# Optimization experiments

Hardware: AMD Instinct MI355X
Metric: run time of the kernel (lower is better)

The kernel has to match this reference:

```python
import jax, jax.numpy as jnp
import numpy as np

B, DIM, NX, NY = 4, 64, 256, 256
HEADS, DIM_HEAD, LATENT, DIM_OUT, KM = 4, 32, 128, 64, 2
DH = DIM_HEAD * KM  # LowRankKernel head dim (also RoPE dim) = 64
EPS = 1e-5
MIN_FREQ = 1.0 / 64.0  # RotaryEmbedding default in FactFormer/LNS repo


def _gelu(x):
    return jax.nn.gelu(x, approximate=False)  # torch nn.GELU default (erf)


def _conv1x1(u, w):
    # u: [b,c,h,w], w: [out,c]  (1x1 conv == channel matmul)
    return jnp.einsum('bchw,oc->bohw', u, w)


def _pooling_reducer(x, win, ln_g, ln_b, w1, w2, b2):
    # x: [b, n_keep, n_pool, c] -> Linear, mean-pool over n_pool, LN+FFN
    h = jnp.einsum('bnmc,hc->bnmh', x, win).mean(axis=2)  # [b, n, hid]
    m = h.mean(axis=-1, keepdims=True)
    v = h.var(axis=-1, keepdims=True)
    h = (h - m) / jnp.sqrt(v + EPS) * ln_g + ln_b
    return _gelu(h @ w1.T) @ w2.T + b2  # [b, n, latent]


def _rope_freqs(n):
    pos = jnp.linspace(0.0, 1.0, n) / MIN_FREQ  # scale/min_freq = 64
    inv = 1.0 / (10000.0 ** (jnp.arange(0, DH, 2, dtype=jnp.float32) / DH))
    f = pos[:, None] * inv[None, :]            # [n, DH//2]
    return jnp.concatenate([f, f], axis=-1)    # [n, DH]


def _apply_rope(x, f):
    # rotate_half = cat(-x2, x1) on half-split (FactFormer convention)
    d = x.shape[-1] // 2
    rot = jnp.concatenate([-x[..., d:], x[..., :d]], axis=-1)
    return x * jnp.cos(f) + rot * jnp.sin(f)


def _low_rank_kernel(x, wqk):
    # x: [b, n, latent] -> K: [b, heads, n, n]; scaling=1, dropout=Identity, qk_norm=False
    b, n, _ = x.shape
    qk = x @ wqk.T
    q, k = jnp.split(qk, 2, axis=-1)
    q = q.reshape(b, n, HEADS, DH).transpose(0, 2, 1, 3)
    k = k.reshape(b, n, HEADS, DH).transpose(0, 2, 1, 3)
    f = _rope_freqs(n)
    q = _apply_rope(q, f)
    k = _apply_rope(k, f)
    return jnp.einsum('bhid,bhjd->bhij', q, k)


def _forward(u, gn_w, gn_b, w_in_proj, w_to_in,
             px_win, px_ln_g, px_ln_b, px_w1, px_w2, px_b2,
             py_win, py_ln_g, py_ln_b, py_w1, py_w2, py_b2,
             kx_wqk, ky_wqk, out_w1, out_w2):
    # GroupNorm(1, dim): normalize over (C,H,W) per sample, affine
    m = u.mean(axis=(1, 2, 3), keepdims=True)
    v = u.var(axis=(1, 2, 3), keepdims=True)
    un = (u - m) / jnp.sqrt(v + EPS) * gn_w[None, :, None, None] + gn_b[None, :, None, None]
    u_phi = _conv1x1(un, w_in_proj)  # [b, heads*dim_head, nx, ny]
    ui = _conv1x1(un, w_to_in)       # [b, dim, nx, ny]
    # to_x: pool over ny -> tokens along nx; to_y: pool over nx -> tokens along ny
    ux = _pooling_reducer(ui.transpose(0, 2, 3, 1), px_win, px_ln_g, px_ln_b, px_w1, px_w2, px_b2)  # [b, nx, latent]
    uy = _pooling_reducer(ui.transpose(0, 3, 2, 1), py_win, py_ln_g, py_ln_b, py_w1, py_w2, py_b2)  # [b, ny, latent]
    kx = _low_rank_kernel(ux, kx_wqk)  # [b, h, nx, nx]
    ky = _low_rank_kernel(uy, ky_wqk)  # [b, h, ny, ny]
    b, hc, nx, ny = u_phi.shape
    up = u_phi.reshape(b, HEADS, hc // HEADS, nx, ny)
    up = jnp.einsum('bhij,bhcjm->bhcim', kx, up)
    up = jnp.einsum('bhlm,bhcim->bhcil', ky, up)
    up = up.reshape(b, hc, nx, ny)
    # InstanceNorm2d (no affine, no running stats)
    m2 = up.mean(axis=(2, 3), keepdims=True)
    v2 = up.var(axis=(2, 3), keepdims=True)
    upn = (up - m2) / jnp.sqrt(v2 + EPS)
    out = _conv1x1(_gelu(_conv1x1(upn, out_w1)), out_w2)
    return out + u


def setup_inputs() -> dict:
    key = jax.random.key(0)
    ks = jax.random.split(key, 16)
    def w(k, shape, s=0.02):
        return (jax.random.normal(k, shape) * s).astype(jnp.float32)
    return {
        'u': jax.random.normal(ks[0], (B, DIM, NX, NY), dtype=jnp.float32),
        'gn_w': jnp.ones((DIM,), jnp.float32), 'gn_b': jnp.zeros((DIM,), jnp.float32),
        'w_in_proj': w(ks[1], (HEADS * DIM_HEAD, DIM)),
        'w_to_in': w(ks[2], (DIM, DIM)),
        'px_win': w(ks[3], (DIM, DIM)),
        'px_ln_g': jnp.ones((DIM,), jnp.float32), 'px_ln_b': jnp.zeros((DIM,), jnp.float32),
        'px_w1': w(ks[4], (2 * DIM, DIM)), 'px_w2': w(ks[5], (LATENT, 2 * DIM)),
        'px_b2': jnp.zeros((LATENT,), jnp.float32),
        'py_win': w(ks[6], (DIM, DIM)),
        'py_ln_g': jnp.ones((DIM,), jnp.float32), 'py_ln_b': jnp.zeros((DIM,), jnp.float32),
        'py_w1': w(ks[7], (2 * DIM, DIM)), 'py_w2': w(ks[8], (LATENT, 2 * DIM)),
        'py_b2': jnp.zeros((LATENT,), jnp.float32),
        'kx_wqk': w(ks[9], (2 * HEADS * DH, LATENT)),
        'ky_wqk': w(ks[10], (2 * HEADS * DH, LATENT)),
        'out_w1': w(ks[11], (DIM_OUT, HEADS * DIM_HEAD)),
        'out_w2': w(ks[12], (DIM_OUT, DIM_OUT)),
    }


def reference(u, gn_w, gn_b, w_in_proj, w_to_in,
              px_win, px_ln_g, px_ln_b, px_w1, px_w2, px_b2,
              py_win, py_ln_g, py_ln_b, py_w1, py_w2, py_b2,
              kx_wqk, ky_wqk, out_w1, out_w2):
    return _forward(u, gn_w, gn_b, w_in_proj, w_to_in,
                    px_win, px_ln_g, px_ln_b, px_w1, px_w2, px_b2,
                    py_win, py_ln_g, py_ln_b, py_w1, py_w2, py_b2,
                    kx_wqk, ky_wqk, out_w1, out_w2)
```

## Files before the change

kernel.cpp:

```cpp
#include <hip/hip_runtime.h>
#include <math.h>

typedef unsigned short ushort_t;
typedef unsigned int uint_t;
typedef __attribute__((ext_vector_type(8))) short s8v;
typedef __attribute__((ext_vector_type(4))) float f4;

#define NPIX 65536
#define EPS_ 1e-5f

__device__ __forceinline__ float bf2f(ushort_t u){ return __uint_as_float(((uint_t)u)<<16); }
__device__ __forceinline__ ushort_t f2bf(float f){
  uint_t u = __float_as_uint(f);
  uint_t r = (u + 0x7fffu + ((u>>16)&1u)) >> 16;
  return (ushort_t)r;
}
__device__ __forceinline__ float bflo(uint_t p){ return __uint_as_float(p<<16); }
__device__ __forceinline__ float bfhi(uint_t p){ return __uint_as_float(p & 0xffff0000u); }
__device__ __forceinline__ uint_t packbf(float a, float b){ return (uint_t)f2bf(a) | ((uint_t)f2bf(b)<<16); }

__device__ __forceinline__ f4 MFMA(s8v a, s8v b, f4 c){
  return __builtin_amdgcn_mfma_f32_16x16x32_bf16(a, b, c, 0, 0, 0);
}

__device__ __forceinline__ float wave_sum(float v){
  #pragma unroll
  for(int m=32;m>=1;m>>=1) v += __shfl_xor(v, m, 64);
  return v;
}

__global__ __launch_bounds__(256) void k1_stats(const float* __restrict__ u,
    float* __restrict__ part, float* __restrict__ pc, float* __restrict__ poolx){
  int blk = blockIdx.x; int b = blk>>8; int c = (blk>>2)&63; int iq = blk&3;
  int t = threadIdx.x; int lane = t&63; int w = t>>6;
  const float* up = u + ((size_t)(b*64+c))*NPIX + iq*64*256;
  __shared__ float red[8];
  float cs=0.f, ss=0.f;
  for(int r=0;r<64;r++){
    float v = up[r*256 + t];
    cs += v; ss += v*v;
  }
  pc[((b*64+c)*4 + iq)*256 + t] = cs;
  float a1 = wave_sum(cs), a2 = wave_sum(ss);
  if(lane==0){ red[w]=a1; red[4+w]=a2; }
  __syncthreads();
  if(t==0){
    part[((b*64+c)*4+iq)*2]   = red[0]+red[1]+red[2]+red[3];
    part[((b*64+c)*4+iq)*2+1] = red[4]+red[5]+red[6]+red[7];
  }
  int r = t>>2, ck = t&3;
  const float* rp = up + r*256 + ck*64;
  float s=0.f;
  #pragma unroll 4
  for(int j=0;j<16;j++){
    float4 v4 = *(const float4*)(rp + j*4);
    s += v4.x + v4.y + v4.z + v4.w;
  }
  s += __shfl_xor(s, 1, 64);
  s += __shfl_xor(s, 2, 64);
  if(ck==0) poolx[(b*256 + iq*64 + r)*64 + c] = s * (1.f/256.f);
}

__global__ void k2_fin(const float* __restrict__ part, float* __restrict__ gnmv){
  int t = threadIdx.x; int b = t>>6; int i = t&63;
  float S1=0.f, S2=0.f;
  #pragma unroll
  for(int q=0;q<4;q++){
    S1 += part[((b*64+i)*4+q)*2];
    S2 += part[((b*64+i)*4+q)*2+1];
  }
  S1 = wave_sum(S1); S2 = wave_sum(S2);
  if(i==0){
    const float inv = 1.f/4194304.f;
    float m = S1*inv; float v = S2*inv - m*m;
    gnmv[b*2] = m; gnmv[b*2+1] = rsqrtf(v + EPS_);
  }
}

__global__ __launch_bounds__(256) void k2b_pool(const float* __restrict__ pc,
    float* __restrict__ pooly){
  int blk = blockIdx.x; int b = blk>>6; int c = blk&63;
  int t = threadIdx.x;
  const float* p = pc + ((size_t)(b*64+c))*4*256 + t;
  float s = p[0] + p[256] + p[512] + p[768];
  pooly[(b*256+t)*64 + c] = s * (1.f/256.f);
}

__global__ __launch_bounds__(256) void k8a_fold(const float* __restrict__ gnmv,
    const float* __restrict__ gnw, const float* __restrict__ gnb,
    const float* __restrict__ w_in_proj, const float* __restrict__ out_w2,
    ushort_t* __restrict__ wpb, float* __restrict__ c0g, ushort_t* __restrict__ w2b){
  int b = blockIdx.x; int t = threadIdx.x;
  __shared__ float scs[64], shs[64];
  if(t<64){
    float mean = gnmv[b*2], rstd = gnmv[b*2+1];
    float sc = rstd*gnw[t];
    scs[t] = sc; shs[t] = gnb[t] - mean*sc;
  }
  __syncthreads();
  int oc = t>>1, h = t&1;
  float c0 = 0.f;
  for(int k=0;k<32;k++){
    int ch = h*32 + k;
    float wv = w_in_proj[oc*64 + ch];
    wpb[((size_t)b*128 + oc)*64 + ch] = f2bf(wv*scs[ch]);
    c0 += wv*shs[ch];
  }
  c0 += __shfl_xor(c0, 1, 64);
  if(h==0) c0g[b*128 + oc] = c0;
  if(b==0){
    for(int e=t;e<4096;e+=256) w2b[e] = f2bf(out_w2[e]);
  }
}

__global__ void k8b_fold(const float* __restrict__ istat,
    const float* __restrict__ out_w1, ushort_t* __restrict__ W1b,
    float* __restrict__ bias1){
  int b = blockIdx.x; int t = threadIdx.x;
  __shared__ float ms[128], rss[128];
  ms[t] = istat[(b*128+t)*2];       rss[t] = istat[(b*128+t)*2+1];
  ms[64+t] = istat[(b*128+64+t)*2]; rss[64+t] = istat[(b*128+64+t)*2+1];
  __syncthreads();
  float bias = 0.f;
  for(int ch=0;ch<128;ch++){
    float wv = out_w1[t*128 + ch];
    float wr = wv*rss[ch];
    W1b[((size_t)b*64 + t)*128 + ch] = f2bf(wr);
    bias += wr*ms[ch];
  }
  bias1[b*64 + t] = bias;
}

__global__ __launch_bounds__(128) void k3_reduce(
    const float* __restrict__ poolx, const float* __restrict__ pooly,
    const float* __restrict__ gnmv,
    const float* __restrict__ gnw, const float* __restrict__ gnb,
    const float* __restrict__ w_to_in,
    const float* __restrict__ xwin, const float* __restrict__ xlg, const float* __restrict__ xlb,
    const float* __restrict__ xw1, const float* __restrict__ xw2, const float* __restrict__ xb2,
    const float* __restrict__ ywin, const float* __restrict__ ylg, const float* __restrict__ ylb,
    const float* __restrict__ yw1, const float* __restrict__ yw2, const float* __restrict__ yb2,
    float* __restrict__ ux, float* __restrict__ uy){
  int id = blockIdx.x;
  int side = id >> 10; int r = id & 1023; int b = r>>8; int i = r&255;
  const float* pool = side ? pooly : poolx;
  const float* win = side ? ywin : xwin;
  const float* lg  = side ? ylg  : xlg;
  const float* lb  = side ? ylb  : xlb;
  const float* w1  = side ? yw1  : xw1;
  const float* w2  = side ? yw2  : xw2;
  const float* b2  = side ? yb2  : xb2;
  float* outp = side ? uy : ux;
  int t = threadIdx.x;
  __shared__ float pn[64], t1[64], hh[64], f1[128];
  float mean = gnmv[b*2], rstd = gnmv[b*2+1];
  if(t<64){
    float pv = pool[(b*256+i)*64 + t];
    pn[t] = (pv - mean)*rstd*gnw[t] + gnb[t];
  }
  __syncthreads();
  if(t<64){
    float acc=0.f; const float* wr = w_to_in + t*64;
    #pragma unroll 8
    for(int c=0;c<64;c++) acc += pn[c]*wr[c];
    t1[t]=acc;
  }
  __syncthreads();
  if(t<64){
    float acc=0.f; const float* wr = win + t*64;
    #pragma unroll 8
    for(int c=0;c<64;c++) acc += t1[c]*wr[c];
    hh[t]=acc;
  }
  __syncthreads();
  if(t<64){
    float v = hh[t];
    float s = wave_sum(v);
    float ss = wave_sum(v*v);
    float m2 = s*(1.f/64.f);
    float var = ss*(1.f/64.f) - m2*m2;
    float rs2 = rsqrtf(var + EPS_);
    hh[t] = (v - m2)*rs2*lg[t] + lb[t];
  }
  __syncthreads();
  {
    float acc=0.f; const float* wr = w1 + t*64;
    #pragma unroll 8
    for(int c=0;c<64;c++) acc += hh[c]*wr[c];
    f1[t] = 0.5f*acc*(1.f + erff(acc*0.70710678118654752f));
  }
  __syncthreads();
  {
    float acc=0.f; const float* wr = w2 + t*128;
    #pragma unroll 8
    for(int j=0;j<128;j++) acc += f1[j]*wr[j];
    outp[(b*256+i)*128 + t] = acc + b2[t];
  }
}

__global__ __launch_bounds__(256) void k4_gemm(
    const float* __restrict__ ux, const float* __restrict__ uy,
    const float* __restrict__ wqkx, const float* __restrict__ wqky,
    ushort_t* __restrict__ qxb, ushort_t* __restrict__ kxTb,
    ushort_t* __restrict__ qyb, ushort_t* __restrict__ kyTb){
  int blk = blockIdx.x;
  int nt = blk&3; int mt = (blk>>2)&1; int b = (blk>>3)&3; int side = blk>>5;
  const float* x  = (side? uy:ux) + (size_t)(b*256 + mt*128)*128;
  const float* wq = (side? wqky:wqkx) + (size_t)nt*128*128;
  ushort_t* qb  = side? qyb : qxb;
  ushort_t* kTb = side? kyTb : kxTb;

  __shared__ __align__(16) ushort_t sA[128*136];
  __shared__ __align__(16) ushort_t sB[128*136];

  int t = threadIdx.x; int lane = t&63; int w = t>>6; int lr = lane&15; int lg = lane>>4;
  for(int e=t;e<4096;e+=256){
    int row = e>>5, c4 = (e&31)*4;
    float4 v = *(const float4*)(x + row*128 + c4);
    uint2 pk; pk.x = packbf(v.x,v.y); pk.y = packbf(v.z,v.w);
    *(uint2*)&sA[row*136 + c4] = pk;
    float4 wv = *(const float4*)(wq + row*128 + c4);
    uint2 wk; wk.x = packbf(wv.x,wv.y); wk.y = packbf(wv.z,wv.w);
    *(uint2*)&sB[row*136 + c4] = wk;
  }
  __syncthreads();
  const f4 fz = {0.f,0.f,0.f,0.f};
  f4 acc[2][8];
  #pragma unroll
  for(int it=0;it<2;it++)
    #pragma unroll
    for(int n2=0;n2<8;n2++) acc[it][n2]=fz;
  #pragma unroll
  for(int kc=0;kc<4;kc++){
    s8v bf[8];
    #pragma unroll
    for(int n2=0;n2<8;n2++)
      bf[n2] = *(const s8v*)&sB[(n2*16+lr)*136 + kc*32 + lg*8];
    #pragma unroll
    for(int it=0;it<2;it++){
      s8v a = *(const s8v*)&sA[(w*32+it*16+lr)*136 + kc*32 + lg*8];
      #pragma unroll
      for(int n2=0;n2<8;n2++)
        acc[it][n2] = MFMA(a, bf[n2], acc[it][n2]);
    }
  }
  if(nt < 2){
    #pragma unroll
    for(int it=0;it<2;it++){
      #pragma unroll
      for(int n2=0;n2<8;n2++){
        int o = nt*128 + n2*16 + lr;
        int h = o>>6, dd = o&63, t32 = dd&31;
        float invf = expf(-(float)t32*(9.210340371976184f/32.f));
        size_t base = (size_t)(b*4+h)*16384;
        #pragma unroll
        for(int r=0;r<4;r++){
          int i = mt*128 + w*32 + it*16 + lg*4 + r;
          float f = (64.f/255.f)*(float)i*invf;
          float sn, cs; __sincosf(f, &sn, &cs);
          float pair = acc[it][n2^2][r];
          float rot = ((n2&2)==0)? -pair : pair;
          float v = acc[it][n2][r]*cs + rot*sn;
          qb[base + (size_t)i*64 + dd] = f2bf(v);
        }
      }
    }
  } else {
    __syncthreads();
    #pragma unroll
    for(int it=0;it<2;it++){
      #pragma unroll
      for(int n2=0;n2<8;n2++){
        int ol = n2*16 + lr;
        int o = nt*128 + ol;
        int t32 = o&31;
        float invf = expf(-(float)t32*(9.210340371976184f/32.f));
        #pragma unroll
        for(int r=0;r<4;r++){
          int il = w*32 + it*16 + lg*4 + r;
          int i = mt*128 + il;
          float f = (64.f/255.f)*(float)i*invf;
          float sn, cs; __sincosf(f, &sn, &cs);
          float pair = acc[it][n2^2][r];
          float rot = ((n2&2)==0)? -pair : pair;
          float v = acc[it][n2][r]*cs + rot*sn;
          sA[ol*136 + il] = f2bf(v);
        }
      }
    }
    __syncthreads();
    {
      int row = t>>1, half = t&1;
      int h = (nt-2)*2 + (row>>6), dd = row&63;
      ushort_t* dst = kTb + (size_t)(b*4+h)*16384 + (size_t)dd*256 + mt*128 + half*64;
      const ushort_t* src = &sA[row*136 + half*64];
      #pragma unroll
      for(int j=0;j<8;j++)
        *(uint4*)(dst + j*8) = *(const uint4*)(src + j*8);
    }
  }
}

__global__ __launch_bounds__(256) void k5s_sums(const ushort_t* __restrict__ kxTb,
    const ushort_t* __restrict__ kyTb, float* __restrict__ ksum){
  int bh = blockIdx.x; int t = threadIdx.x;
  int row = t>>2, g = t&3;
  const ushort_t* kx = kxTb + (size_t)bh*16384 + row*256 + g*64;
  float s = 0.f;
  #pragma unroll
  for(int j=0;j<8;j++){
    uint4 v = *(const uint4*)(kx + j*8);
    s += bflo(v.x)+bfhi(v.x)+bflo(v.y)+bfhi(v.y)+bflo(v.z)+bfhi(v.z)+bflo(v.w)+bfhi(v.w);
  }
  s += __shfl_xor(s,1,64); s += __shfl_xor(s,2,64);
  if(g==0) ksum[bh*128 + row] = s;
  const ushort_t* ky = kyTb + (size_t)bh*16384 + row*256 + g*64;
  float s2 = 0.f;
  #pragma unroll
  for(int j=0;j<8;j++){
    uint4 v = *(const uint4*)(ky + j*8);
    s2 += bflo(v.x)+bfhi(v.x)+bflo(v.y)+bfhi(v.y)+bflo(v.z)+bfhi(v.z)+bflo(v.w)+bfhi(v.w);
  }
  s2 += __shfl_xor(s2,1,64); s2 += __shfl_xor(s2,2,64);
  if(g==0) ksum[bh*128 + 64 + row] = s2;
}

__global__ __launch_bounds__(512) void k7a_core(
    const float* __restrict__ u,
    const ushort_t* __restrict__ kxTb, const ushort_t* __restrict__ kyTb,
    ushort_t* __restrict__ Cb){
  int blk = blockIdx.x; int b = blk>>6;
  const float* up = u + (size_t)blk*NPIX;
  __shared__ __align__(16) ushort_t su[2][64*264];
  __shared__ __align__(16) ushort_t sT1[4][64*68];
  int t = threadIdx.x; int w = t>>6; int lane = t&63; int lr = lane&15; int lg = lane>>4;
  int h = w>>1, sub = w&1;
  const ushort_t* KyT = kyTb + (size_t)(b*4+h)*16384;
  const ushort_t* KxT = kxTb + (size_t)(b*4+h)*16384;
  const f4 fz = {0.f,0.f,0.f,0.f};
  f4 cacc[2][4];
  #pragma unroll
  for(int it=0;it<2;it++)
    #pragma unroll
    for(int et=0;et<4;et++) cacc[it][et]=fz;

  auto stageld = [&](int jc, int buf){
    #pragma unroll
    for(int k=0;k<8;k++){
      int flat = k*512 + t;
      int row = flat>>6, col4 = flat&63;
      float4 v = *(const float4*)(up + (size_t)(jc*64+row)*256 + col4*4);
      uint2 pk; pk.x = packbf(v.x,v.y); pk.y = packbf(v.z,v.w);
      *(uint2*)&su[buf][row*264 + col4*4] = pk;
    }
  };
  stageld(0, 0);
  __syncthreads();
  for(int jc=0;jc<4;jc++){
    int cur = jc&1;
    f4 acc[2][4];
    #pragma unroll
    for(int jt=0;jt<2;jt++)
      #pragma unroll
      for(int et=0;et<4;et++) acc[jt][et]=fz;
    #pragma unroll
    for(int km=0;km<8;km++){
      s8v a0 = *(const s8v*)&su[cur][(sub*32+lr)*264 + km*32 + lg*8];
      s8v a1 = *(const s8v*)&su[cur][(sub*32+16+lr)*264 + km*32 + lg*8];
      #pragma unroll
      for(int et=0;et<4;et++){
        s8v bv = *(const s8v*)(KyT + (et*16+lr)*256 + km*32 + lg*8);
        acc[0][et] = MFMA(a0,bv,acc[0][et]);
        acc[1][et] = MFMA(a1,bv,acc[1][et]);
      }
    }
    #pragma unroll
    for(int jt=0;jt<2;jt++)
      #pragma unroll
      for(int et=0;et<4;et++){
        f4 v = acc[jt][et];
        uint2 pk; pk.x=packbf(v.x,v.y); pk.y=packbf(v.z,v.w);
        *(uint2*)&sT1[h][(et*16+lr)*68 + sub*32 + jt*16 + lg*4] = pk;
      }
    __syncthreads();
    if(jc<3) stageld(jc+1, cur^1);
    #pragma unroll
    for(int kj=0;kj<2;kj++){
      s8v a0 = *(const s8v*)(KxT + (size_t)(sub*32+lr)*256 + jc*64 + kj*32 + lg*8);
      s8v a1 = *(const s8v*)(KxT + (size_t)(sub*32+16+lr)*256 + jc*64 + kj*32 + lg*8);
      #pragma unroll
      for(int et=0;et<4;et++){
        s8v bv = *(const s8v*)&sT1[h][(et*16+lr)*68 + kj*32 + lg*8];
        cacc[0][et] = MFMA(a0,bv,cacc[0][et]);
        cacc[1][et] = MFMA(a1,bv,cacc[1][et]);
      }
    }
    __syncthreads();
  }
  ushort_t* cbase = Cb + ((size_t)blk*4 + h)*4096;
  #pragma unroll
  for(int it=0;it<2;it++)
    #pragma unroll
    for(int et=0;et<4;et++){
      f4 v = cacc[it][et];
      uint2 pk; pk.x=packbf(v.x,v.y); pk.y=packbf(v.z,v.w);
      *(uint2*)&cbase[(et*16+lr)*64 + sub*32 + it*16 + lg*4] = pk;
    }
}

__global__ __launch_bounds__(256) void k7m_mix(
    const ushort_t* __restrict__ Cb, const ushort_t* __restrict__ wpb,
    const float* __restrict__ c0g, const float* __restrict__ ksum,
    ushort_t* __restrict__ cT){
  int blk = blockIdx.x; int bh = blk>>4; int et = blk&15;
  int b = bh>>2, h = bh&3;
  __shared__ __align__(16) ushort_t sC[64*264];
  __shared__ float sWf[32*64];
  __shared__ float sKx[64], sKy4[4];
  int t = threadIdx.x;
  #pragma unroll
  for(int k=0;k<8;k++){
    int flat = k*256 + t;
    int ic = flat>>5, q = flat&31;
    uint4 v = *(const uint4*)(Cb + ((size_t)(b*64+ic)*4 + h)*4096 + et*256 + q*8);
    *(uint4*)&sC[ic*264 + q*8] = v;
  }
  for(int e=t;e<2048;e+=256){
    int ch = e>>6, ic = e&63;
    sWf[e] = bf2f(wpb[((size_t)b*128 + h*32 + ch)*64 + ic]);
  }
  if(t<64) sKx[t] = ksum[bh*128 + t];
  if(t<4)  sKy4[t] = ksum[bh*128 + 64 + et*4 + t];
  __syncthreads();
  int chg = t>>5, edq = t&31, ed0 = edq*8;
  float c0v[4];
  #pragma unroll
  for(int cc=0;cc<4;cc++) c0v[cc] = c0g[b*128 + h*32 + chg*4 + cc];
  float acc[4][8];
  #pragma unroll
  for(int j=0;j<8;j++){
    int ed = ed0 + j;
    float r1 = sKy4[ed>>6]*sKx[ed&63];
    #pragma unroll
    for(int cc=0;cc<4;cc++) acc[cc][j] = c0v[cc]*r1;
  }
  for(int ic=0;ic<64;ic++){
    uint4 cv = *(const uint4*)&sC[ic*264 + ed0];
    float x[8];
    x[0]=bflo(cv.x); x[1]=bfhi(cv.x); x[2]=bflo(cv.y); x[3]=bfhi(cv.y);
    x[4]=bflo(cv.z); x[5]=bfhi(cv.z); x[6]=bflo(cv.w); x[7]=bfhi(cv.w);
    #pragma unroll
    for(int cc=0;cc<4;cc++){
      float wv = sWf[(chg*4+cc)*64 + ic];
      #pragma unroll
      for(int j=0;j<8;j++) acc[cc][j] += wv*x[j];
    }
  }
  #pragma unroll
  for(int cc=0;cc<4;cc++){
    uint2 p0, p1;
    p0.x = packbf(acc[cc][0],acc[cc][1]); p0.y = packbf(acc[cc][2],acc[cc][3]);
    p1.x = packbf(acc[cc][4],acc[cc][5]); p1.y = packbf(acc[cc][6],acc[cc][7]);
    ushort_t* dst = cT + ((size_t)bh*32 + chg*4+cc)*4096 + et*256 + ed0;
    *(uint2*)(dst) = p0;
    *(uint2*)(dst+4) = p1;
  }
}

__global__ __launch_bounds__(256) void k7b_heavy(
    const ushort_t* __restrict__ cT,
    const ushort_t* __restrict__ qxb, const ushort_t* __restrict__ qyb,
    ushort_t* __restrict__ up2, float* __restrict__ istat){
  int blk = blockIdx.x;
  int c = blk & 31; int h = (blk>>5)&3; int b = blk>>7;
  int bh = b*4 + h; int ch = h*32 + c;
  const ushort_t* Qx  = qxb + (size_t)bh*16384;
  const ushort_t* Qy  = qyb + (size_t)bh*16384;
  const ushort_t* cTc = cT + (size_t)(bh*32 + c)*4096;
  ushort_t* out_c = up2 + (size_t)(b*128 + ch)*NPIX;

  __shared__ __align__(16) ushort_t sP[256*72];
  __shared__ float sRed[8];

  int t = threadIdx.x; int w = t>>6; int lane = t&63; int lr = lane&15; int lg = lane>>4;
  const f4 fz = {0.f,0.f,0.f,0.f};
  {
    s8v aF[4][2];
    #pragma unroll
    for(int me=0;me<4;me++)
      #pragma unroll
      for(int kd=0;kd<2;kd++)
        aF[me][kd] = *(const s8v*)(cTc + (me*16+lr)*64 + kd*32 + lg*8);
    #pragma unroll
    for(int it=0;it<4;it++){
      s8v b0 = *(const s8v*)(Qx + (w*64+it*16+lr)*64 + lg*8);
      s8v b1 = *(const s8v*)(Qx + (w*64+it*16+lr)*64 + 32 + lg*8);
      #pragma unroll
      for(int me=0;me<4;me++){
        f4 pv = MFMA(aF[me][0], b0, fz);
        pv = MFMA(aF[me][1], b1, pv);
        uint2 pk; pk.x=packbf(pv.x,pv.y); pk.y=packbf(pv.z,pv.w);
        *(uint2*)&sP[(w*64+it*16+lr)*72 + me*16 + lg*4] = pk;
      }
    }
  }
  __syncthreads();
  float lsum=0.f, lssq=0.f;
  {
    s8v aP[4][2];
    #pragma unroll
    for(int it=0;it<4;it++)
      #pragma unroll
      for(int ke=0;ke<2;ke++)
        aP[it][ke] = *(const s8v*)&sP[(w*64+it*16+lr)*72 + ke*32 + lg*8];
    for(int lt=0;lt<4;lt++){
      s8v bq[4][2];
      #pragma unroll
      for(int nt=0;nt<4;nt++)
        #pragma unroll
        for(int ke=0;ke<2;ke++)
          bq[nt][ke] = *(const s8v*)(Qy + (lt*64+nt*16+lr)*64 + ke*32 + lg*8);
      #pragma unroll
      for(int it=0;it<4;it++){
        #pragma unroll
        for(int nt=0;nt<4;nt++){
          f4 o = MFMA(bq[nt][0], aP[it][0], fz);
          o = MFMA(bq[nt][1], aP[it][1], o);
          lsum += o[0]+o[1]+o[2]+o[3];
          lssq += o[0]*o[0]+o[1]*o[1]+o[2]*o[2]+o[3]*o[3];
          uint2 pk; pk.x = packbf(o[0],o[1]); pk.y = packbf(o[2],o[3]);
          *(uint2*)(out_c + (size_t)(w*64 + it*16 + lr)*256 + lt*64 + nt*16 + lg*4) = pk;
        }
      }
    }
  }
  float a1 = wave_sum(lsum), a2 = wave_sum(lssq);
  if(lane==0){ sRed[w]=a1; sRed[4+w]=a2; }
  __syncthreads();
  if(t==0){
    float S = sRed[0]+sRed[1]+sRed[2]+sRed[3];
    float SS = sRed[4]+sRed[5]+sRed[6]+sRed[7];
    float m = S*(1.f/65536.f);
    float var = SS*(1.f/65536.f) - m*m;
    istat[(b*128+ch)*2] = m;
    istat[(b*128+ch)*2+1] = rsqrtf(var + EPS_);
  }
}

__global__ __launch_bounds__(256) void kf_out(
    const ushort_t* __restrict__ up2, const ushort_t* __restrict__ W1b,
    const float* __restrict__ bias1, const ushort_t* __restrict__ w2b,
    const float* __restrict__ u, float* __restrict__ out){
  int blk = blockIdx.x;
  int b = blk>>9; int pix0 = (blk&511)<<7;
  __shared__ __align__(16) unsigned char smraw[128*132*2];
  ushort_t* sX = (ushort_t*)smraw;
  ushort_t* sG = (ushort_t*)smraw;
  float* sO = (float*)smraw;
  int t = threadIdx.x; int lane = t&63; int w = t>>6; int lr = lane&15; int lg = lane>>4;
  {
    int ch = t>>4; int px = (t&15)*8;
    #pragma unroll
    for(int it=0; it<8; it++){
      int c = it*16 + ch;
      uint4 v = *(const uint4*)(up2 + ((size_t)(b*128+c))*NPIX + pix0 + px);
      uint2 lo; lo.x = v.x; lo.y = v.y;
      uint2 hi; hi.x = v.z; hi.y = v.w;
      *(uint2*)&sX[c*132 + px] = lo;
      *(uint2*)&sX[c*132 + px + 4] = hi;
    }
  }
  __syncthreads();
  const ushort_t* w1p = W1b + (size_t)b*64*128;
  f4 g[2][4];
  #pragma unroll
  for(int it=0;it<2;it++)
    #pragma unroll
    for(int nt=0;nt<4;nt++){
      float bv = -bias1[b*64 + nt*16 + lr];
      f4 ci = {bv,bv,bv,bv};
      g[it][nt] = ci;
    }
  #pragma unroll
  for(int kc=0;kc<4;kc++){
    s8v bf[4];
    #pragma unroll
    for(int nt=0;nt<4;nt++)
      bf[nt] = *(const s8v*)(w1p + (nt*16+lr)*128 + kc*32 + lg*8);
    #pragma unroll
    for(int it=0;it<2;it++){
      int pix = w*32 + it*16 + lr;
      s8v a;
      #pragma unroll
      for(int j=0;j<8;j++) a[j] = (short)sX[(kc*32+lg*8+j)*132 + pix];
      #pragma unroll
      for(int nt=0;nt<4;nt++)
        g[it][nt] = MFMA(a, bf[nt], g[it][nt]);
    }
  }
  #pragma unroll
  for(int it=0;it<2;it++)
    #pragma unroll
    for(int nt=0;nt<4;nt++){
      f4 v = g[it][nt];
      #pragma unroll
      for(int r=0;r<4;r++){
        float x = v[r];
        v[r] = 0.5f*x*(1.f + erff(x*0.70710678118654752f));
      }
      g[it][nt] = v;
    }
  __syncthreads();
  #pragma unroll
  for(int it=0;it<2;it++)
    #pragma unroll
    for(int nt=0;nt<4;nt++){
      f4 v = g[it][nt];
      uint2 pk; pk.x = packbf(v.x,v.y); pk.y = packbf(v.z,v.w);
      *(uint2*)&sG[(nt*16+lr)*132 + w*32 + it*16 + lg*4] = pk;
    }
  __syncthreads();
  f4 o2[2][4];
  const f4 fz = {0.f,0.f,0.f,0.f};
  #pragma unroll
  for(int it=0;it<2;it++)
    #pragma unroll
    for(int nt=0;nt<4;nt++) o2[it][nt]=fz;
  #pragma unroll
  for(int kc=0;kc<2;kc++){
    s8v bf[4];
    #pragma unroll
    for(int nt=0;nt<4;nt++)
      bf[nt] = *(const s8v*)(w2b + (nt*16+lr)*64 + kc*32 + lg*8);
    #pragma unroll
    for(int it=0;it<2;it++){
      int pix = w*32 + it*16 + lr;
      s8v a;
      #pragma unroll
      for(int j=0;j<8;j++) a[j] = (short)sG[(kc*32+lg*8+j)*132 + pix];
      #pragma unroll
      for(int nt=0;nt<4;nt++)
        o2[it][nt] = MFMA(a, bf[nt], o2[it][nt]);
    }
  }
  __syncthreads();
  #pragma unroll
  for(int it=0;it<2;it++)
    #pragma unroll
    for(int nt=0;nt<4;nt++)
      *(f4*)&sO[(nt*16+lr)*132 + w*32 + it*16 + lg*4] = o2[it][nt];
  __syncthreads();
  {
    int oc = t>>5; int px = (t&31)*4;
    #pragma unroll
    for(int it=0;it<8;it++){
      int o = it*8 + oc;
      float4 ov = *(const float4*)&sO[o*132 + px];
      float4 uv = *(const float4*)(u + ((size_t)(b*64+o))*NPIX + pix0 + px);
      float4 rv;
      rv.x = ov.x+uv.x; rv.y = ov.y+uv.y; rv.z = ov.z+uv.z; rv.w = ov.w+uv.w;
      *(float4*)(out + ((size_t)(b*64+o))*NPIX + pix0 + px) = rv;
    }
  }
}

extern "C" void kernel_launch(void* const* d_in, const int* in_sizes, int n_in,
                              void* d_out, int out_size, void* d_ws, size_t ws_size,
                              hipStream_t stream) {
  (void)in_sizes; (void)n_in; (void)out_size; (void)ws_size;
  const float* u        = (const float*)d_in[0];
  const float* gnw      = (const float*)d_in[1];
  const float* gnb      = (const float*)d_in[2];
  const float* w_in_proj= (const float*)d_in[3];
  const float* w_to_in  = (const float*)d_in[4];
  const float* px_win   = (const float*)d_in[5];
  const float* px_ln_g  = (const float*)d_in[6];
  const float* px_ln_b  = (const float*)d_in[7];
  const float* px_w1    = (const float*)d_in[8];
  const float* px_w2    = (const float*)d_in[9];
  const float* px_b2    = (const float*)d_in[10];
  const float* py_win   = (const float*)d_in[11];
  const float* py_ln_g  = (const float*)d_in[12];
  const float* py_ln_b  = (const float*)d_in[13];
  const float* py_w1    = (const float*)d_in[14];
  const float* py_w2    = (const float*)d_in[15];
  const float* py_b2    = (const float*)d_in[16];
  const float* kx_wqk   = (const float*)d_in[17];
  const float* ky_wqk   = (const float*)d_in[18];
  const float* out_w1   = (const float*)d_in[19];
  const float* out_w2   = (const float*)d_in[20];
  float* out = (float*)d_out;

  float* fw = (float*)d_ws;
  float* part  = fw + 0;
  float* gnmv  = fw + 2048;
  float* pc    = fw + 4096;
  float* poolx = fw + 266240;
  float* pooly = fw + 331776;
  float* ux    = fw + 397312;
  float* uy    = fw + 528384;
  float* istat = fw + 659456;
  float* c0g   = fw + 660480;
  float* bias1 = fw + 660992;
  ushort_t* wpb = (ushort_t*)(fw + 661504);
  ushort_t* W1b = (ushort_t*)(fw + 677888);
  ushort_t* w2b = (ushort_t*)(fw + 694272);
  float* ksum   = fw + 696320;
  ushort_t* qxb  = (ushort_t*)(fw + 4096);
  ushort_t* kxTb = (ushort_t*)(fw + 135168);
  ushort_t* qyb  = (ushort_t*)(fw + 698368);
  ushort_t* kyTb = (ushort_t*)(fw + 829440);
  ushort_t* up2  = (ushort_t*)(fw + 960512);
  ushort_t* Cb = (ushort_t*)d_out;
  ushort_t* cT = (ushort_t*)d_out + 4194304;

  k1_stats<<<dim3(1024), dim3(256), 0, stream>>>(u, part, pc, poolx);
  k2_fin<<<dim3(1), dim3(256), 0, stream>>>(part, gnmv);
  k2b_pool<<<dim3(256), dim3(256), 0, stream>>>(pc, pooly);
  k8a_fold<<<dim3(4), dim3(256), 0, stream>>>(gnmv, gnw, gnb, w_in_proj, out_w2, wpb, c0g, w2b);
  k3_reduce<<<dim3(2048), dim3(128), 0, stream>>>(poolx, pooly, gnmv, gnw, gnb, w_to_in,
      px_win, px_ln_g, px_ln_b, px_w1, px_w2, px_b2,
      py_win, py_ln_g, py_ln_b, py_w1, py_w2, py_b2, ux, uy);
  k4_gemm<<<dim3(64), dim3(256), 0, stream>>>(ux, uy, kx_wqk, ky_wqk, qxb, kxTb, qyb, kyTb);
  k5s_sums<<<dim3(16), dim3(256), 0, stream>>>(kxTb, kyTb, ksum);
  k7a_core<<<dim3(256), dim3(512), 0, stream>>>(u, kxTb, kyTb, Cb);
  k7m_mix<<<dim3(256), dim3(256), 0, stream>>>(Cb, wpb, c0g, ksum, cT);
  k7b_heavy<<<dim3(512), dim3(256), 0, stream>>>(cT, qxb, qyb, up2, istat);
  k8b_fold<<<dim3(4), dim3(64), 0, stream>>>(istat, out_w1, W1b, bias1);
  kf_out<<<dim3(2048), dim3(256), 0, stream>>>(up2, W1b, bias1, w2b, u, out);
}
```

Baseline: 210.5 us.

## Split k7a_core reduction over two blocks per channel, sum partials in k7m_mix

```diff
diff --git a/kernel.cpp b/kernel.cpp
--- a/kernel.cpp
+++ b/kernel.cpp
@@ -329,9 +329,9 @@
     const float* __restrict__ u,
     const ushort_t* __restrict__ kxTb, const ushort_t* __restrict__ kyTb,
     ushort_t* __restrict__ Cb){
-  int blk = blockIdx.x; int b = blk>>6;
-  const float* up = u + (size_t)blk*NPIX;
-  __shared__ __align__(16) ushort_t su[2][64*264];
+  int blk = blockIdx.x; int b = blk>>7; int ch = (blk>>1)&63; int half = blk&1;
+  const float* up = u + (size_t)(b*64+ch)*NPIX;
+  __shared__ __align__(16) ushort_t su[64*264];
   __shared__ __align__(16) ushort_t sT1[4][64*68];
   int t = threadIdx.x; int w = t>>6; int lane = t&63; int lr = lane&15; int lg = lane>>4;
   int h = w>>1, sub = w&1;
@@ -344,20 +344,17 @@
     #pragma unroll
     for(int et=0;et<4;et++) cacc[it][et]=fz;
 
-  auto stageld = [&](int jc, int buf){
+  for(int jcl=0;jcl<2;jcl++){
+    int jc = half*2 + jcl;
     #pragma unroll
     for(int k=0;k<8;k++){
       int flat = k*512 + t;
       int row = flat>>6, col4 = flat&63;
       float4 v = *(const float4*)(up + (size_t)(jc*64+row)*256 + col4*4);
       uint2 pk; pk.x = packbf(v.x,v.y); pk.y = packbf(v.z,v.w);
-      *(uint2*)&su[buf][row*264 + col4*4] = pk;
-    }
-  };
-  stageld(0, 0);
-  __syncthreads();
-  for(int jc=0;jc<4;jc++){
-    int cur = jc&1;
+      *(uint2*)&su[row*264 + col4*4] = pk;
+    }
+    __syncthreads();
     f4 acc[2][4];
     #pragma unroll
     for(int jt=0;jt<2;jt++)
@@ -365,8 +362,8 @@
       for(int et=0;et<4;et++) acc[jt][et]=fz;
     #pragma unroll
     for(int km=0;km<8;km++){
-      s8v a0 = *(const s8v*)&su[cur][(sub*32+lr)*264 + km*32 + lg*8];
-      s8v a1 = *(const s8v*)&su[cur][(sub*32+16+lr)*264 + km*32 + lg*8];
+      s8v a0 = *(const s8v*)&su[(sub*32+lr)*264 + km*32 + lg*8];
+      s8v a1 = *(const s8v*)&su[(sub*32+16+lr)*264 + km*32 + lg*8];
       #pragma unroll
       for(int et=0;et<4;et++){
         s8v bv = *(const s8v*)(KyT + (et*16+lr)*256 + km*32 + lg*8);
@@ -383,7 +380,6 @@
         *(uint2*)&sT1[h][(et*16+lr)*68 + sub*32 + jt*16 + lg*4] = pk;
       }
     __syncthreads();
-    if(jc<3) stageld(jc+1, cur^1);
     #pragma unroll
     for(int kj=0;kj<2;kj++){
       s8v a0 = *(const s8v*)(KxT + (size_t)(sub*32+lr)*256 + jc*64 + kj*32 + lg*8);
@@ -395,7 +391,6 @@
         cacc[1][et] = MFMA(a1,bv,cacc[1][et]);
       }
     }
-    __syncthreads();
   }
   ushort_t* cbase = Cb + ((size_t)blk*4 + h)*4096;
   #pragma unroll
@@ -414,17 +409,9 @@
     ushort_t* __restrict__ cT){
   int blk = blockIdx.x; int bh = blk>>4; int et = blk&15;
   int b = bh>>2, h = bh&3;
-  __shared__ __align__(16) ushort_t sC[64*264];
   __shared__ float sWf[32*64];
   __shared__ float sKx[64], sKy4[4];
   int t = threadIdx.x;
-  #pragma unroll
-  for(int k=0;k<8;k++){
-    int flat = k*256 + t;
-    int ic = flat>>5, q = flat&31;
-    uint4 v = *(const uint4*)(Cb + ((size_t)(b*64+ic)*4 + h)*4096 + et*256 + q*8);
-    *(uint4*)&sC[ic*264 + q*8] = v;
-  }
   for(int e=t;e<2048;e+=256){
     int ch = e>>6, ic = e&63;
     sWf[e] = bf2f(wpb[((size_t)b*128 + h*32 + ch)*64 + ic]);
@@ -445,10 +432,14 @@
     for(int cc=0;cc<4;cc++) acc[cc][j] = c0v[cc]*r1;
   }
   for(int ic=0;ic<64;ic++){
-    uint4 cv = *(const uint4*)&sC[ic*264 + ed0];
+    const ushort_t* p = Cb + ((((size_t)(b*64+ic))*2)*4 + h)*4096 + et*256 + ed0;
+    uint4 v0 = *(const uint4*)p;
+    uint4 v1 = *(const uint4*)(p + 16384);
     float x[8];
-    x[0]=bflo(cv.x); x[1]=bfhi(cv.x); x[2]=bflo(cv.y); x[3]=bfhi(cv.y);
-    x[4]=bflo(cv.z); x[5]=bfhi(cv.z); x[6]=bflo(cv.w); x[7]=bfhi(cv.w);
+    x[0]=bflo(v0.x)+bflo(v1.x); x[1]=bfhi(v0.x)+bfhi(v1.x);
+    x[2]=bflo(v0.y)+bflo(v1.y); x[3]=bfhi(v0.y)+bfhi(v1.y);
+    x[4]=bflo(v0.z)+bflo(v1.z); x[5]=bfhi(v0.z)+bfhi(v1.z);
+    x[6]=bflo(v0.w)+bflo(v1.w); x[7]=bfhi(v0.w)+bfhi(v1.w);
     #pragma unroll
     for(int cc=0;cc<4;cc++){
       float wv = sWf[(chg*4+cc)*64 + ic];
@@ -712,7 +703,7 @@
   ushort_t* kyTb = (ushort_t*)(fw + 829440);
   ushort_t* up2  = (ushort_t*)(fw + 960512);
   ushort_t* Cb = (ushort_t*)d_out;
-  ushort_t* cT = (ushort_t*)d_out + 4194304;
+  ushort_t* cT = (ushort_t*)d_out + 8388608;
 
   k1_stats<<<dim3(1024), dim3(256), 0, stream>>>(u, part, pc, poolx);
   k2_fin<<<dim3(1), dim3(256), 0, stream>>>(part, gnmv);
@@ -723,7 +714,7 @@
       py_win, py_ln_g, py_ln_b, py_w1, py_w2, py_b2, ux, uy);
   k4_gemm<<<dim3(64), dim3(256), 0, stream>>>(ux, uy, kx_wqk, ky_wqk, qxb, kxTb, qyb, kyTb);
   k5s_sums<<<dim3(16), dim3(256), 0, stream>>>(kxTb, kyTb, ksum);
-  k7a_core<<<dim3(256), dim3(512), 0, stream>>>(u, kxTb, kyTb, Cb);
+  k7a_core<<<dim3(512), dim3(512), 0, stream>>>(u, kxTb, kyTb, Cb);
   k7m_mix<<<dim3(256), dim3(256), 0, stream>>>(Cb, wpb, c0g, ksum, cT);
   k7b_heavy<<<dim3(512), dim3(256), 0, stream>>>(cT, qxb, qyb, up2, istat);
   k8b_fold<<<dim3(4), dim3(64), 0, stream>>>(istat, out_w1, W1b, bias1);
```

New measurement: 226.6 us. 1.08x slower.
